# Optimization experiments

Measured on AMD Instinct MI355X. Metric: run time of the kernel, lower is better.

The kernel has to match this reference:

```python
import jax, jax.numpy as jnp
import numpy as np
from jax import lax

CHUNK = 64
KEY_DIM = 128
SCALE = KEY_DIM ** -0.5  # query scaling
EPS = 1e-06


def setup_inputs() -> dict:
    key = jax.random.key(0)
    ks = jax.random.split(key, 5)
    B, H, S, Dk, Dv = 2, 16, 4096, 128, 256
    q = jax.random.normal(ks[0], (B, H, S, Dk), jnp.float32)
    k = jax.random.normal(ks[1], (B, H, S, Dk), jnp.float32)
    v = jax.random.normal(ks[2], (B, H, S, Dv), jnp.float32)
    # decay log-gate: small negative values
    g = -0.1 * jax.random.uniform(ks[3], (B, H, S), jnp.float32)
    # delta-rule learning rate in (0, 1)
    beta = 0.05 + 0.9 * jax.random.uniform(ks[4], (B, H, S), jnp.float32)
    return {"q": q, "k": k, "v": v, "g": g, "beta": beta}


def _chunkwise(q, k, v, g, beta):
    B, H, S, Dk = q.shape
    Dv = v.shape[-1]
    L = CHUNK
    N = S // L  # S chosen as multiple of CHUNK (pad branch is a no-op)
    # L2-normalize q, k
    q = q / (jnp.linalg.norm(q, axis=-1, keepdims=True) + EPS)
    k = k / (jnp.linalg.norm(k, axis=-1, keepdims=True) + EPS)
    # chunk and move chunk axis to front for scan: [N, B, H, L, D]
    qc = jnp.transpose(q.reshape(B, H, N, L, Dk), (2, 0, 1, 3, 4))
    kc = jnp.transpose(k.reshape(B, H, N, L, Dk), (2, 0, 1, 3, 4))
    vc = jnp.transpose(v.reshape(B, H, N, L, Dv), (2, 0, 1, 3, 4))
    gc = jnp.transpose(g.reshape(B, H, N, L), (2, 0, 1, 3))
    bc = jnp.transpose(beta.reshape(B, H, N, L), (2, 0, 1, 3))

    eye = jnp.eye(L, dtype=jnp.float32)
    mask_lower = jnp.tril(jnp.ones((L, L), jnp.float32), k=-1)
    causal_mask = jnp.tril(jnp.ones((L, L), jnp.float32))

    def process_chunk(S_state, chunk_inputs):
        q_c, k_c, v_c, g_c, beta_c = chunk_inputs
        g_cum = jnp.cumsum(g_c, axis=-1)                     # [B,H,L]
        g_total = g_cum[..., -1]                             # [B,H]
        relative_gate = jnp.exp(g_cum[..., None, :] - g_cum[..., :, None])  # [B,H,L,L]
        kk = jnp.einsum('bhik,bhjk->bhij', k_c, k_c)
        M = kk * relative_gate * mask_lower
        A = eye + beta_c[..., None] * M
        diag_beta = eye * beta_c[..., None]
        T = lax.linalg.triangular_solve(A, diag_beta, left_side=True, lower=True)
        g_cum_exp = jnp.exp(g_cum)[..., None]                # [B,H,L,1]
        k_gated = k_c * g_cum_exp
        v_gated = v_c * g_cum_exp
        W = jnp.einsum('bhij,bhjk->bhik', T, k_gated)
        U = jnp.einsum('bhij,bhjv->bhiv', T, v_gated)
        O_inter = jnp.einsum('bhik,bhkv->bhiv', q_c, S_state) * g_cum_exp
        WS = jnp.einsum('bhik,bhkv->bhiv', W, S_state)
        correction = U - WS
        qk = jnp.einsum('bhik,bhjk->bhij', q_c, k_c)
        qk_gated = qk * causal_mask * relative_gate
        O_intra = jnp.einsum('bhij,bhjv->bhiv', qk_gated * SCALE, correction)
        O_chunk = O_inter * SCALE + O_intra
        S_new = S_state * jnp.exp(g_total)[..., None, None] + \
            jnp.einsum('bhik,bhiv->bhkv', k_gated, correction)
        return S_new, O_chunk

    S0 = jnp.zeros((B, H, Dk, Dv), dtype=jnp.float32)
    final_state, outputs = lax.scan(process_chunk, S0, (qc, kc, vc, gc, bc))
    output = jnp.transpose(outputs, (1, 2, 0, 3, 4)).reshape(B, H, S, Dv)
    return output.astype(q.dtype), final_state


def reference(q, k, v, g, beta):
    return _chunkwise(q, k, v, g, beta)
```

## Files before the change

### kernel.cpp

```cpp
#include <hip/hip_runtime.h>
#include <math.h>


namespace {

constexpr int kBH = 32;
constexpr int kS = 4096;
constexpr int kDk = 128;
constexpr int kDv = 256;
constexpr int kL = 64;
constexpr int kNC = kS / kL;
constexpr int kThreads = 512;
constexpr float kScale = 0.08838834764831845f;
constexpr float kEps = 1e-6f;

constexpr int KST = 136;
constexpr int TST = 72;
constexpr int SBT = 136;
constexpr int AS  = 68;

typedef __attribute__((ext_vector_type(8))) short short8;
typedef __attribute__((ext_vector_type(4))) short short4v;
typedef __attribute__((ext_vector_type(4))) float f32x4;

__device__ __forceinline__ short f2bf(float f) {
  union { float f; unsigned u; } x;
  x.f = f;
  unsigned r = x.u + 0x7fffu + ((x.u >> 16) & 1u);
  return (short)(r >> 16);
}

#define MFMA16(a, b, c) __builtin_amdgcn_mfma_f32_16x16x32_bf16((a), (b), (c), 0, 0, 0)

__global__ __launch_bounds__(kThreads, 2)
void gdn_mfma_kernel(const float* __restrict__ q, const float* __restrict__ k,
                     const float* __restrict__ v, const float* __restrict__ g,
                     const float* __restrict__ beta, float* __restrict__ out) {
  __shared__ short sKp[kL][KST];
  __shared__ short sKm[kL][KST];
  __shared__ short sQp[kL][KST];
  __shared__ short sQm[kL][KST];
  __shared__ short sTb[kL][TST];
  __shared__ short sAqk[kL][TST];
  __shared__ short sSb[32][SBT];
  __shared__ short sYT[32][TST];
  __shared__ short sCT[32][TST];
  __shared__ float sA[kL][AS];
  __shared__ float sVinv[4][16][17];
  __shared__ float sTmp[32][33];
  __shared__ float sGexp[kL], sGinv[kL], sBeta[kL];

  const int t = threadIdx.x;
  const int wave = t >> 6;
  const int lane = t & 63;
  const int n16 = lane & 15;
  const int quad = lane >> 4;
  const int r2 = t >> 3;
  const int c8 = t & 7;

  const int bh = blockIdx.x & 31;
  const int vb = blockIdx.x >> 5;

  const float* qp_g = q + (size_t)bh * kS * kDk;
  const float* kp_g = k + (size_t)bh * kS * kDk;
  const float* vp_g = v + (size_t)bh * kS * kDv + vb * 32;
  const float* gp_g = g + (size_t)bh * kS;
  const float* bp_g = beta + (size_t)bh * kS;
  float* op_g = out + (size_t)bh * kS * kDv + vb * 32;
  float* sp_g = out + (size_t)kBH * kS * kDv + (size_t)bh * kDk * kDv + vb * 32;

  for (int i = t; i < kL * TST; i += kThreads) { (&sTb[0][0])[i] = 0; (&sAqk[0][0])[i] = 0; }
  for (int i = t; i < 32 * SBT; i += kThreads) (&sSb[0][0])[i] = 0;

  f32x4 Sacc[4];
  Sacc[0] = 0; Sacc[1] = 0; Sacc[2] = 0; Sacc[3] = 0;

  for (int n = 0; n < kNC; ++n) {
    __syncthreads();

    float kv[16], qv[16], rk, rq;
    {
      const float* krow = kp_g + (size_t)(n * kL + r2) * kDk + c8 * 16;
      const float* qrow = qp_g + (size_t)(n * kL + r2) * kDk + c8 * 16;
      float ssk = 0.f, ssq = 0.f;
      #pragma unroll
      for (int m = 0; m < 4; ++m) {
        const float4 a = reinterpret_cast<const float4*>(krow)[m];
        const float4 b = reinterpret_cast<const float4*>(qrow)[m];
        kv[4*m+0]=a.x; kv[4*m+1]=a.y; kv[4*m+2]=a.z; kv[4*m+3]=a.w;
        qv[4*m+0]=b.x; qv[4*m+1]=b.y; qv[4*m+2]=b.z; qv[4*m+3]=b.w;
        ssk += a.x*a.x + a.y*a.y + a.z*a.z + a.w*a.w;
        ssq += b.x*b.x + b.y*b.y + b.z*b.z + b.w*b.w;
      }
      #pragma unroll
      for (int off = 4; off >= 1; off >>= 1) {
        ssk += __shfl_xor(ssk, off, 8);
        ssq += __shfl_xor(ssq, off, 8);
      }
      rk = 1.f / (sqrtf(ssk) + kEps);
      rq = 1.f / (sqrtf(ssq) + kEps);
    }
    if (t < kL) {
      float gv = gp_g[n * kL + t];
      float bt = bp_g[n * kL + t];
      #pragma unroll
      for (int off = 1; off < 64; off <<= 1) {
        float up = __shfl_up(gv, off, 64);
        if (lane >= off) gv += up;
      }
      sGexp[t] = __expf(gv);
      sGinv[t] = __expf(-gv);
      sBeta[t] = bt;
    }
    __syncthreads();

    {
      const float ge = sGexp[r2], gi = sGinv[r2];
      const float m_kp = rk * ge, m_km = rk * gi;
      const float m_qp = rq * ge * kScale, m_qm = rq * gi * kScale;
      short8 w0, w1;
      #pragma unroll
      for (int m = 0; m < 8; ++m) { w0[m] = f2bf(kv[m] * m_kp); w1[m] = f2bf(kv[8+m] * m_kp); }
      *(short8*)&sKp[r2][c8*16] = w0; *(short8*)&sKp[r2][c8*16+8] = w1;
      #pragma unroll
      for (int m = 0; m < 8; ++m) { w0[m] = f2bf(kv[m] * m_km); w1[m] = f2bf(kv[8+m] * m_km); }
      *(short8*)&sKm[r2][c8*16] = w0; *(short8*)&sKm[r2][c8*16+8] = w1;
      #pragma unroll
      for (int m = 0; m < 8; ++m) { w0[m] = f2bf(qv[m] * m_qp); w1[m] = f2bf(qv[8+m] * m_qp); }
      *(short8*)&sQp[r2][c8*16] = w0; *(short8*)&sQp[r2][c8*16+8] = w1;
      #pragma unroll
      for (int m = 0; m < 8; ++m) { w0[m] = f2bf(qv[m] * m_qm); w1[m] = f2bf(qv[8+m] * m_qm); }
      *(short8*)&sQm[r2][c8*16] = w0; *(short8*)&sQm[r2][c8*16+8] = w1;
    }
    __syncthreads();

    {
      const int jmax = wave & 3;
      const int i0 = (wave & 3) * 16;
      const short (*Asrc)[KST] = (wave < 4) ? sKm : sQm;
      f32x4 acc[4];
      acc[0] = 0; acc[1] = 0; acc[2] = 0; acc[3] = 0;
      #pragma unroll
      for (int ks = 0; ks < 4; ++ks) {
        short8 af = *(const short8*)&Asrc[i0 + n16][ks*32 + quad*8];
        for (int jt = 0; jt <= jmax; ++jt) {
          short8 bf = *(const short8*)&sKp[jt*16 + n16][ks*32 + quad*8];
          acc[jt] = MFMA16(af, bf, acc[jt]);
        }
      }
      if (wave < 4) {
        #pragma unroll
        for (int reg = 0; reg < 4; ++reg) {
          const int i = i0 + quad*4 + reg;
          const float bi = sBeta[i];
          for (int jt = 0; jt <= jmax; ++jt) {
            const int j = jt*16 + n16;
            if (j < i) sA[i][j] = bi * acc[jt][reg];
          }
        }
      } else {
        for (int jt = 0; jt <= jmax; ++jt) {
          #pragma unroll
          for (int reg = 0; reg < 4; ++reg) {
            const int i = i0 + quad*4 + reg, j = jt*16 + n16;
            sAqk[i][j] = (j <= i) ? f2bf(acc[jt][reg]) : (short)0;
          }
        }
      }
    }
    __syncthreads();

    f32x4 yacc[2], oacc[2];
    float vv[2][4];
    const int iy0 = (wave & 3) * 16;
    auto py_step = [&](int ks) {
      short8 ak = *(const short8*)&sKp[iy0 + n16][ks*32 + quad*8];
      short8 aq = *(const short8*)&sQp[iy0 + n16][ks*32 + quad*8];
      #pragma unroll
      for (int vt = 0; vt < 2; ++vt) {
        short8 bs = *(const short8*)&sSb[vt*16 + n16][ks*32 + quad*8];
        yacc[vt] = MFMA16(ak, bs, yacc[vt]);
        oacc[vt] = MFMA16(aq, bs, oacc[vt]);
      }
    };

    if (wave >= 4) {
      yacc[0] = 0; yacc[1] = 0; oacc[0] = 0; oacc[1] = 0;
      #pragma unroll
      for (int vt = 0; vt < 2; ++vt)
        #pragma unroll
        for (int reg = 0; reg < 4; ++reg)
          vv[vt][reg] = vp_g[(size_t)(n*kL + iy0 + quad*4 + reg) * kDv + vt*16 + n16];
      py_step(0);
    } else if (t < 64) {
      const int I = t >> 4, c = t & 15;
      float x[16];
      #pragma unroll
      for (int i = 0; i < 16; ++i) {
        float xi = (i == c) ? 1.f : 0.f;
        for (int j = 0; j < i; ++j) xi -= sA[I*16 + i][I*16 + j] * x[j];
        x[i] = xi;
      }
      const float bc = sBeta[I*16 + c];
      #pragma unroll
      for (int i = 0; i < 16; ++i) {
        sVinv[I][i][c] = x[i];
        sTb[I*16 + i][I*16 + c] = f2bf(x[i] * bc);
      }
    }
    __syncthreads();

    if (wave >= 4) {
      py_step(1);
    } else {
      const int r = t >> 4, c = t & 15;
      float m1 = 0.f, m3 = 0.f;
      #pragma unroll
      for (int kk = 0; kk < 16; ++kk) {
        m1 += sVinv[1][r][kk] * sA[16 + kk][c];
        m3 += sVinv[3][r][kk] * sA[48 + kk][32 + c];
      }
      sTmp[r][c] = m1;
      sTmp[16 + r][c] = m3;
    }
    __syncthreads();

    if (wave >= 4) {
      py_step(2);
    } else {
      const int r = t >> 4, c = t & 15;
      float x1 = 0.f, x3 = 0.f;
      #pragma unroll
      for (int kk = 0; kk < 16; ++kk) {
        x1 += sTmp[r][kk] * sVinv[0][kk][c];
        x3 += sTmp[16 + r][kk] * sVinv[2][kk][c];
      }
      x1 = -x1; x3 = -x3;
      sA[16 + r][c] = x1;
      sTb[16 + r][c] = f2bf(x1 * sBeta[c]);
      sA[48 + r][32 + c] = x3;
      sTb[48 + r][32 + c] = f2bf(x3 * sBeta[32 + c]);
    }
    __syncthreads();

    if (wave >= 4) {
      py_step(3);
    } else {
      #pragma unroll
      for (int p = 0; p < 4; ++p) {
        const int idx = t + 256*p;
        const int r = idx >> 5, c = idx & 31;
        float m = 0.f;
        if (c < 16) {
          #pragma unroll
          for (int kk = 0; kk < 16; ++kk) m += sA[32 + r][kk] * sVinv[0][kk][c];
          #pragma unroll
          for (int kk = 16; kk < 32; ++kk) m += sA[32 + r][kk] * sA[kk][c];
        } else {
          #pragma unroll
          for (int kk = 16; kk < 32; ++kk) m += sA[32 + r][kk] * sVinv[1][kk - 16][c - 16];
        }
        sTmp[r][c] = m;
      }
    }
    __syncthreads();

    if (wave >= 4) {
      #pragma unroll
      for (int vt = 0; vt < 2; ++vt) {
        short4v yw;
        #pragma unroll
        for (int reg = 0; reg < 4; ++reg) {
          const float gei = sGexp[iy0 + quad*4 + reg];
          yw[reg] = f2bf(gei * vv[vt][reg] - yacc[vt][reg]);
        }
        *(short4v*)&sYT[vt*16 + n16][iy0 + quad*4] = yw;
      }
    } else {
      #pragma unroll
      for (int p = 0; p < 4; ++p) {
        const int idx = t + 256*p;
        const int r = idx >> 5, c = idx & 31;
        float xv = 0.f;
        if (r < 16) {
          #pragma unroll
          for (int kk = 0; kk < 16; ++kk) xv += sVinv[2][r][kk] * sTmp[kk][c];
        } else {
          #pragma unroll
          for (int kk = 0; kk < 16; ++kk) xv += sA[32 + r][32 + kk] * sTmp[kk][c];
          #pragma unroll
          for (int kk = 16; kk < 32; ++kk) xv += sVinv[3][r - 16][kk - 16] * sTmp[kk][c];
        }
        sTb[32 + r][c] = f2bf(-xv * sBeta[c]);
      }
    }
    __syncthreads();

    {
      const int ic0 = (wave >> 1) * 16, vc0 = (wave & 1) * 16;
      f32x4 cacc; cacc = 0;
      #pragma unroll
      for (int ks = 0; ks < 2; ++ks) {
        short8 af = *(const short8*)&sTb[ic0 + n16][ks*32 + quad*8];
        short8 bf = *(const short8*)&sYT[vc0 + n16][ks*32 + quad*8];
        cacc = MFMA16(af, bf, cacc);
      }
      short4v cw;
      #pragma unroll
      for (int reg = 0; reg < 4; ++reg) cw[reg] = f2bf(cacc[reg]);
      *(short4v*)&sCT[vc0 + n16][ic0 + quad*4] = cw;
    }
    __syncthreads();

    if (wave >= 4) {
      const int io = (wave & 3) * 16;
      #pragma unroll
      for (int ks = 0; ks < 2; ++ks) {
        short8 af = *(const short8*)&sAqk[io + n16][ks*32 + quad*8];
        #pragma unroll
        for (int vt = 0; vt < 2; ++vt) {
          short8 bf = *(const short8*)&sCT[vt*16 + n16][ks*32 + quad*8];
          oacc[vt] = MFMA16(af, bf, oacc[vt]);
        }
      }
      #pragma unroll
      for (int vt = 0; vt < 2; ++vt)
        #pragma unroll
        for (int reg = 0; reg < 4; ++reg)
          op_g[(size_t)(n*kL + io + quad*4 + reg) * kDv + vt*16 + n16] = oacc[vt][reg];
    } else {
      const float decay = sGexp[kL - 1];
      Sacc[0] *= decay; Sacc[1] *= decay; Sacc[2] *= decay; Sacc[3] *= decay;
      #pragma unroll
      for (int a = 0; a < 2; ++a) {
        const int d0 = (wave & 3) * 32 + a * 16;
        #pragma unroll
        for (int ks = 0; ks < 2; ++ks) {
          short8 af;
          #pragma unroll
          for (int j = 0; j < 8; ++j) af[j] = sKp[ks*32 + quad*8 + j][d0 + n16];
          #pragma unroll
          for (int b = 0; b < 2; ++b) {
            short8 bf = *(const short8*)&sCT[b*16 + n16][ks*32 + quad*8];
            Sacc[a*2 + b] = MFMA16(af, bf, Sacc[a*2 + b]);
          }
        }
        #pragma unroll
        for (int b = 0; b < 2; ++b) {
          short4v sw;
          #pragma unroll
          for (int reg = 0; reg < 4; ++reg) sw[reg] = f2bf(Sacc[a*2 + b][reg]);
          *(short4v*)&sSb[b*16 + n16][d0 + quad*4] = sw;
        }
      }
    }
  }

  if (wave < 4) {
    #pragma unroll
    for (int a = 0; a < 2; ++a)
      #pragma unroll
      for (int b = 0; b < 2; ++b)
        #pragma unroll
        for (int reg = 0; reg < 4; ++reg) {
          const int d = (wave & 3) * 32 + a * 16 + quad * 4 + reg;
          sp_g[(size_t)d * kDv + b * 16 + n16] = Sacc[a*2 + b][reg];
        }
  }
}

}

extern "C" void kernel_launch(void* const* d_in, const int* in_sizes, int n_in,
                              void* d_out, int out_size, void* d_ws, size_t ws_size,
                              hipStream_t stream) {
  (void)in_sizes; (void)n_in; (void)d_ws; (void)ws_size; (void)out_size;
  const float* q    = (const float*)d_in[0];
  const float* k    = (const float*)d_in[1];
  const float* v    = (const float*)d_in[2];
  const float* g    = (const float*)d_in[3];
  const float* beta = (const float*)d_in[4];
  float* out = (float*)d_out;
  gdn_mfma_kernel<<<dim3(kBH * (kDv / 32)), dim3(kThreads), 0, stream>>>(
      q, k, v, g, beta, out);
}
```

Measured before the change: 957.0 us.

## Split value dimension into 16-wide slices and fold gates into epilogues to shrink LDS

The grid now splits Dv into 16 slices of 16 columns instead of 8 slices of 32, doubling block count, and launch bounds request 4 blocks per CU. Shared memory is cut by dropping the gated K/Q copies (Kp/Km/Qp/Qm). Only normalized K and Q are stored, and the exp(g) factors are applied in the epilogues of the A, Aqk, Y, C and output steps. Scalar arrays are aliased into padding of sA and sU, and one barrier is removed. The intent is higher occupancy and parallelism for the sequential chunk scan, at the cost of recomputing the per-chunk K/Q/T work twice as many times across blocks.

Result: slower. 1.759 ms (+83.8%).

```diff
diff --git a/kernel.cpp b/kernel.cpp
--- a/kernel.cpp
+++ b/kernel.cpp
@@ -11,6 +11,7 @@
 constexpr int kL = 64;
 constexpr int kNC = kS / kL;
 constexpr int kThreads = 512;
+constexpr int kVSlices = 16;
 constexpr float kScale = 0.08838834764831845f;
 constexpr float kEps = 1e-6f;
 
@@ -32,23 +33,25 @@
 
 #define MFMA16(a, b, c) __builtin_amdgcn_mfma_f32_16x16x32_bf16((a), (b), (c), 0, 0, 0)
 
-__global__ __launch_bounds__(kThreads, 2)
+__global__ __launch_bounds__(kThreads, 4)
 void gdn_mfma_kernel(const float* __restrict__ q, const float* __restrict__ k,
                      const float* __restrict__ v, const float* __restrict__ g,
                      const float* __restrict__ beta, float* __restrict__ out) {
-  __shared__ short sKp[kL][KST];
-  __shared__ short sKm[kL][KST];
-  __shared__ short sQp[kL][KST];
-  __shared__ short sQm[kL][KST];
-  __shared__ short sTb[kL][TST];
-  __shared__ short sAqk[kL][TST];
-  __shared__ short sSb[32][SBT];
-  __shared__ short sYT[32][TST];
-  __shared__ short sCT[32][TST];
-  __shared__ float sA[kL][AS];
-  __shared__ float sVinv[4][16][17];
-  __shared__ float sTmp[32][33];
-  __shared__ float sGexp[kL], sGinv[kL], sBeta[kL];
+  __shared__ __align__(16) short sKn[kL][KST];
+  __shared__ __align__(16) short sQn[kL][KST];
+  __shared__ __align__(16) short sTb[kL][TST];
+  __shared__ __align__(16) short sAqk[kL][TST];
+  __shared__ __align__(16) short sSb[16][SBT];
+  __shared__ __align__(16) float sA[kL][AS];
+  __shared__ __align__(16) float sU[1056];
+  __shared__ __align__(16) short sCG[16][TST];
+
+#define GEXPV(i) sA[(i) >> 4][16 + ((i) & 15)]
+#define GINVV(i) sA[4 + ((i) >> 4)][16 + ((i) & 15)]
+#define BETAV(i) sA[8 + ((i) >> 4)][16 + ((i) & 15)]
+#define SVINV(I, i, c) sA[((I) & 1) * 16 + (i)][32 + ((I) >> 1) * 17 + (c)]
+#define STMP(r, c) sU[(r) * 33 + (c)]
+  short* const sYT = (short*)sU;
 
   const int t = threadIdx.x;
   const int wave = t >> 6;
@@ -63,17 +66,19 @@
 
   const float* qp_g = q + (size_t)bh * kS * kDk;
   const float* kp_g = k + (size_t)bh * kS * kDk;
-  const float* vp_g = v + (size_t)bh * kS * kDv + vb * 32;
+  const float* vp_g = v + (size_t)bh * kS * kDv + vb * 16;
   const float* gp_g = g + (size_t)bh * kS;
   const float* bp_g = beta + (size_t)bh * kS;
-  float* op_g = out + (size_t)bh * kS * kDv + vb * 32;
-  float* sp_g = out + (size_t)kBH * kS * kDv + (size_t)bh * kDk * kDv + vb * 32;
+  float* op_g = out + (size_t)bh * kS * kDv + vb * 16;
+  float* sp_g = out + (size_t)kBH * kS * kDv + (size_t)bh * kDk * kDv + vb * 16;
 
   for (int i = t; i < kL * TST; i += kThreads) { (&sTb[0][0])[i] = 0; (&sAqk[0][0])[i] = 0; }
-  for (int i = t; i < 32 * SBT; i += kThreads) (&sSb[0][0])[i] = 0;
-
-  f32x4 Sacc[4];
-  Sacc[0] = 0; Sacc[1] = 0; Sacc[2] = 0; Sacc[3] = 0;
+  for (int i = t; i < 16 * SBT; i += kThreads) (&sSb[0][0])[i] = 0;
+
+  f32x4 Sacc[2];
+  Sacc[0] = 0; Sacc[1] = 0;
+
+  const int iy0 = (wave & 3) * 16;
 
   for (int n = 0; n < kNC; ++n) {
     __syncthreads();
@@ -108,89 +113,82 @@
         float up = __shfl_up(gv, off, 64);
         if (lane >= off) gv += up;
       }
-      sGexp[t] = __expf(gv);
-      sGinv[t] = __expf(-gv);
-      sBeta[t] = bt;
-    }
-    __syncthreads();
-
+      GEXPV(t) = __expf(gv);
+      GINVV(t) = __expf(-gv);
+      BETAV(t) = bt;
+    }
     {
-      const float ge = sGexp[r2], gi = sGinv[r2];
-      const float m_kp = rk * ge, m_km = rk * gi;
-      const float m_qp = rq * ge * kScale, m_qm = rq * gi * kScale;
+      const float mk = rk, mq = rq * kScale;
       short8 w0, w1;
       #pragma unroll
-      for (int m = 0; m < 8; ++m) { w0[m] = f2bf(kv[m] * m_kp); w1[m] = f2bf(kv[8+m] * m_kp); }
-      *(short8*)&sKp[r2][c8*16] = w0; *(short8*)&sKp[r2][c8*16+8] = w1;
-      #pragma unroll
-      for (int m = 0; m < 8; ++m) { w0[m] = f2bf(kv[m] * m_km); w1[m] = f2bf(kv[8+m] * m_km); }
-      *(short8*)&sKm[r2][c8*16] = w0; *(short8*)&sKm[r2][c8*16+8] = w1;
-      #pragma unroll
-      for (int m = 0; m < 8; ++m) { w0[m] = f2bf(qv[m] * m_qp); w1[m] = f2bf(qv[8+m] * m_qp); }
-      *(short8*)&sQp[r2][c8*16] = w0; *(short8*)&sQp[r2][c8*16+8] = w1;
-      #pragma unroll
-      for (int m = 0; m < 8; ++m) { w0[m] = f2bf(qv[m] * m_qm); w1[m] = f2bf(qv[8+m] * m_qm); }
-      *(short8*)&sQm[r2][c8*16] = w0; *(short8*)&sQm[r2][c8*16+8] = w1;
-    }
-    __syncthreads();
-
+      for (int m = 0; m < 8; ++m) { w0[m] = f2bf(kv[m] * mk); w1[m] = f2bf(kv[8+m] * mk); }
+      *(short8*)&sKn[r2][c8*16] = w0; *(short8*)&sKn[r2][c8*16+8] = w1;
+      #pragma unroll
+      for (int m = 0; m < 8; ++m) { w0[m] = f2bf(qv[m] * mq); w1[m] = f2bf(qv[8+m] * mq); }
+      *(short8*)&sQn[r2][c8*16] = w0; *(short8*)&sQn[r2][c8*16+8] = w1;
+    }
+    __syncthreads();
+
+    float vv[4];
     {
       const int jmax = wave & 3;
-      const int i0 = (wave & 3) * 16;
-      const short (*Asrc)[KST] = (wave < 4) ? sKm : sQm;
+      const short (*Asrc)[KST] = (wave < 4) ? sKn : sQn;
       f32x4 acc[4];
       acc[0] = 0; acc[1] = 0; acc[2] = 0; acc[3] = 0;
+      if (wave >= 4) {
+        #pragma unroll
+        for (int reg = 0; reg < 4; ++reg)
+          vv[reg] = vp_g[(size_t)(n*kL + iy0 + quad*4 + reg) * kDv + n16];
+      }
       #pragma unroll
       for (int ks = 0; ks < 4; ++ks) {
-        short8 af = *(const short8*)&Asrc[i0 + n16][ks*32 + quad*8];
+        short8 af = *(const short8*)&Asrc[iy0 + n16][ks*32 + quad*8];
         for (int jt = 0; jt <= jmax; ++jt) {
-          short8 bf = *(const short8*)&sKp[jt*16 + n16][ks*32 + quad*8];
+          short8 bf = *(const short8*)&sKn[jt*16 + n16][ks*32 + quad*8];
           acc[jt] = MFMA16(af, bf, acc[jt]);
         }
       }
       if (wave < 4) {
+        float sc[4];
         #pragma unroll
         for (int reg = 0; reg < 4; ++reg) {
-          const int i = i0 + quad*4 + reg;
-          const float bi = sBeta[i];
-          for (int jt = 0; jt <= jmax; ++jt) {
-            const int j = jt*16 + n16;
-            if (j < i) sA[i][j] = bi * acc[jt][reg];
+          const int i = iy0 + quad*4 + reg;
+          sc[reg] = BETAV(i) * GINVV(i);
+        }
+        for (int jt = 0; jt <= jmax; ++jt) {
+          const int j = jt*16 + n16;
+          const float gej = GEXPV(j);
+          #pragma unroll
+          for (int reg = 0; reg < 4; ++reg) {
+            const int i = iy0 + quad*4 + reg;
+            if (j < i) sA[i][j] = sc[reg] * gej * acc[jt][reg];
           }
         }
       } else {
+        float gi[4];
+        #pragma unroll
+        for (int reg = 0; reg < 4; ++reg) gi[reg] = GINVV(iy0 + quad*4 + reg);
         for (int jt = 0; jt <= jmax; ++jt) {
           #pragma unroll
           for (int reg = 0; reg < 4; ++reg) {
-            const int i = i0 + quad*4 + reg, j = jt*16 + n16;
-            sAqk[i][j] = (j <= i) ? f2bf(acc[jt][reg]) : (short)0;
+            const int i = iy0 + quad*4 + reg, j = jt*16 + n16;
+            sAqk[i][j] = (j <= i) ? f2bf(acc[jt][reg] * gi[reg]) : (short)0;
           }
         }
       }
     }
     __syncthreads();
 
-    f32x4 yacc[2], oacc[2];
-    float vv[2][4];
-    const int iy0 = (wave & 3) * 16;
+    f32x4 yacc = 0, oacc = 0;
     auto py_step = [&](int ks) {
-      short8 ak = *(const short8*)&sKp[iy0 + n16][ks*32 + quad*8];
-      short8 aq = *(const short8*)&sQp[iy0 + n16][ks*32 + quad*8];
-      #pragma unroll
-      for (int vt = 0; vt < 2; ++vt) {
-        short8 bs = *(const short8*)&sSb[vt*16 + n16][ks*32 + quad*8];
-        yacc[vt] = MFMA16(ak, bs, yacc[vt]);
-        oacc[vt] = MFMA16(aq, bs, oacc[vt]);
-      }
+      short8 ak = *(const short8*)&sKn[iy0 + n16][ks*32 + quad*8];
+      short8 aq = *(const short8*)&sQn[iy0 + n16][ks*32 + quad*8];
+      short8 bs = *(const short8*)&sSb[n16][ks*32 + quad*8];
+      yacc = MFMA16(ak, bs, yacc);
+      oacc = MFMA16(aq, bs, oacc);
     };
 
     if (wave >= 4) {
-      yacc[0] = 0; yacc[1] = 0; oacc[0] = 0; oacc[1] = 0;
-      #pragma unroll
-      for (int vt = 0; vt < 2; ++vt)
-        #pragma unroll
-        for (int reg = 0; reg < 4; ++reg)
-          vv[vt][reg] = vp_g[(size_t)(n*kL + iy0 + quad*4 + reg) * kDv + vt*16 + n16];
       py_step(0);
     } else if (t < 64) {
       const int I = t >> 4, c = t & 15;
@@ -201,10 +199,10 @@
         for (int j = 0; j < i; ++j) xi -= sA[I*16 + i][I*16 + j] * x[j];
         x[i] = xi;
       }
-      const float bc = sBeta[I*16 + c];
+      const float bc = BETAV(I*16 + c);
       #pragma unroll
       for (int i = 0; i < 16; ++i) {
-        sVinv[I][i][c] = x[i];
+        SVINV(I, i, c) = x[i];
         sTb[I*16 + i][I*16 + c] = f2bf(x[i] * bc);
       }
     }
@@ -217,11 +215,11 @@
       float m1 = 0.f, m3 = 0.f;
       #pragma unroll
       for (int kk = 0; kk < 16; ++kk) {
-        m1 += sVinv[1][r][kk] * sA[16 + kk][c];
-        m3 += sVinv[3][r][kk] * sA[48 + kk][32 + c];
-      }
-      sTmp[r][c] = m1;
-      sTmp[16 + r][c] = m3;
+        m1 += SVINV(1, r, kk) * sA[16 + kk][c];
+        m3 += SVINV(3, r, kk) * sA[48 + kk][32 + c];
+      }
+      STMP(r, c) = m1;
+      STMP(16 + r, c) = m3;
     }
     __syncthreads();
 
@@ -232,14 +230,14 @@
       float x1 = 0.f, x3 = 0.f;
       #pragma unroll
       for (int kk = 0; kk < 16; ++kk) {
-        x1 += sTmp[r][kk] * sVinv[0][kk][c];
-        x3 += sTmp[16 + r][kk] * sVinv[2][kk][c];
+        x1 += STMP(r, kk) * SVINV(0, kk, c);
+        x3 += STMP(16 + r, kk) * SVINV(2, kk, c);
       }
       x1 = -x1; x3 = -x3;
       sA[16 + r][c] = x1;
-      sTb[16 + r][c] = f2bf(x1 * sBeta[c]);
+      sTb[16 + r][c] = f2bf(x1 * BETAV(c));
       sA[48 + r][32 + c] = x3;
-      sTb[48 + r][32 + c] = f2bf(x3 * sBeta[32 + c]);
+      sTb[48 + r][32 + c] = f2bf(x3 * BETAV(32 + c));
     }
     __syncthreads();
 
@@ -253,29 +251,29 @@
         float m = 0.f;
         if (c < 16) {
           #pragma unroll
-          for (int kk = 0; kk < 16; ++kk) m += sA[32 + r][kk] * sVinv[0][kk][c];
+          for (int kk = 0; kk < 16; ++kk) m += sA[32 + r][kk] * SVINV(0, kk, c);
           #pragma unroll
           for (int kk = 16; kk < 32; ++kk) m += sA[32 + r][kk] * sA[kk][c];
         } else {
           #pragma unroll
-          for (int kk = 16; kk < 32; ++kk) m += sA[32 + r][kk] * sVinv[1][kk - 16][c - 16];
-        }
-        sTmp[r][c] = m;
-      }
-    }
-    __syncthreads();
-
-    if (wave >= 4) {
-      #pragma unroll
-      for (int vt = 0; vt < 2; ++vt) {
-        short4v yw;
-        #pragma unroll
-        for (int reg = 0; reg < 4; ++reg) {
-          const float gei = sGexp[iy0 + quad*4 + reg];
-          yw[reg] = f2bf(gei * vv[vt][reg] - yacc[vt][reg]);
-        }
-        *(short4v*)&sYT[vt*16 + n16][iy0 + quad*4] = yw;
-      }
+          for (int kk = 16; kk < 32; ++kk) m += sA[32 + r][kk] * SVINV(1, kk - 16, c - 16);
+        }
+        STMP(r, c) = m;
+      }
+    }
+    __syncthreads();
+
+    short4v yw;
+    short8 af2[2];
+    if (wave >= 4) {
+      #pragma unroll
+      for (int reg = 0; reg < 4; ++reg) {
+        const float ge = GEXPV(iy0 + quad*4 + reg);
+        yw[reg] = f2bf(ge * (vv[reg] - yacc[reg]));
+        oacc[reg] *= ge;
+      }
+      af2[0] = *(const short8*)&sAqk[iy0 + n16][quad*8];
+      af2[1] = *(const short8*)&sAqk[iy0 + n16][32 + quad*8];
     } else {
       #pragma unroll
       for (int p = 0; p < 4; ++p) {
@@ -284,74 +282,75 @@
         float xv = 0.f;
         if (r < 16) {
           #pragma unroll
-          for (int kk = 0; kk < 16; ++kk) xv += sVinv[2][r][kk] * sTmp[kk][c];
+          for (int kk = 0; kk < 16; ++kk) xv += SVINV(2, r, kk) * STMP(kk, c);
         } else {
           #pragma unroll
-          for (int kk = 0; kk < 16; ++kk) xv += sA[32 + r][32 + kk] * sTmp[kk][c];
-          #pragma unroll
-          for (int kk = 16; kk < 32; ++kk) xv += sVinv[3][r - 16][kk - 16] * sTmp[kk][c];
-        }
-        sTb[32 + r][c] = f2bf(-xv * sBeta[c]);
-      }
-    }
-    __syncthreads();
-
-    {
-      const int ic0 = (wave >> 1) * 16, vc0 = (wave & 1) * 16;
-      f32x4 cacc; cacc = 0;
-      #pragma unroll
-      for (int ks = 0; ks < 2; ++ks) {
-        short8 af = *(const short8*)&sTb[ic0 + n16][ks*32 + quad*8];
-        short8 bf = *(const short8*)&sYT[vc0 + n16][ks*32 + quad*8];
-        cacc = MFMA16(af, bf, cacc);
-      }
-      short4v cw;
-      #pragma unroll
-      for (int reg = 0; reg < 4; ++reg) cw[reg] = f2bf(cacc[reg]);
-      *(short4v*)&sCT[vc0 + n16][ic0 + quad*4] = cw;
-    }
-    __syncthreads();
-
-    if (wave >= 4) {
-      const int io = (wave & 3) * 16;
-      #pragma unroll
-      for (int ks = 0; ks < 2; ++ks) {
-        short8 af = *(const short8*)&sAqk[io + n16][ks*32 + quad*8];
-        #pragma unroll
-        for (int vt = 0; vt < 2; ++vt) {
-          short8 bf = *(const short8*)&sCT[vt*16 + n16][ks*32 + quad*8];
-          oacc[vt] = MFMA16(af, bf, oacc[vt]);
-        }
-      }
-      #pragma unroll
-      for (int vt = 0; vt < 2; ++vt)
-        #pragma unroll
-        for (int reg = 0; reg < 4; ++reg)
-          op_g[(size_t)(n*kL + io + quad*4 + reg) * kDv + vt*16 + n16] = oacc[vt][reg];
-    } else {
-      const float decay = sGexp[kL - 1];
-      Sacc[0] *= decay; Sacc[1] *= decay; Sacc[2] *= decay; Sacc[3] *= decay;
-      #pragma unroll
-      for (int a = 0; a < 2; ++a) {
-        const int d0 = (wave & 3) * 32 + a * 16;
+          for (int kk = 0; kk < 16; ++kk) xv += sA[32 + r][32 + kk] * STMP(kk, c);
+          #pragma unroll
+          for (int kk = 16; kk < 32; ++kk) xv += SVINV(3, r - 16, kk - 16) * STMP(kk, c);
+        }
+        sTb[32 + r][c] = f2bf(-xv * BETAV(c));
+      }
+    }
+    __syncthreads();
+
+    short8 afr[2][2];
+    if (wave >= 4) {
+      *(short4v*)&sYT[n16*TST + iy0 + quad*4] = yw;
+    } else {
+      const int d0b = (wave & 3) * 32;
+      #pragma unroll
+      for (int a = 0; a < 2; ++a)
         #pragma unroll
         for (int ks = 0; ks < 2; ++ks) {
           short8 af;
           #pragma unroll
-          for (int j = 0; j < 8; ++j) af[j] = sKp[ks*32 + quad*8 + j][d0 + n16];
-          #pragma unroll
-          for (int b = 0; b < 2; ++b) {
-            short8 bf = *(const short8*)&sCT[b*16 + n16][ks*32 + quad*8];
-            Sacc[a*2 + b] = MFMA16(af, bf, Sacc[a*2 + b]);
-          }
-        }
-        #pragma unroll
-        for (int b = 0; b < 2; ++b) {
-          short4v sw;
-          #pragma unroll
-          for (int reg = 0; reg < 4; ++reg) sw[reg] = f2bf(Sacc[a*2 + b][reg]);
-          *(short4v*)&sSb[b*16 + n16][d0 + quad*4] = sw;
-        }
+          for (int j = 0; j < 8; ++j)
+            af[j] = sKn[ks*32 + quad*8 + j][d0b + a*16 + n16];
+          afr[a][ks] = af;
+        }
+    }
+    __syncthreads();
+
+    if (wave < 4) {
+      f32x4 cacc = 0;
+      #pragma unroll
+      for (int ks = 0; ks < 2; ++ks) {
+        short8 af = *(const short8*)&sTb[iy0 + n16][ks*32 + quad*8];
+        short8 bf = *(const short8*)&sYT[n16*TST + ks*32 + quad*8];
+        cacc = MFMA16(af, bf, cacc);
+      }
+      short4v cw;
+      #pragma unroll
+      for (int reg = 0; reg < 4; ++reg)
+        cw[reg] = f2bf(cacc[reg] * GEXPV(iy0 + quad*4 + reg));
+      *(short4v*)&sCG[n16][iy0 + quad*4] = cw;
+    }
+    __syncthreads();
+
+    if (wave >= 4) {
+      #pragma unroll
+      for (int ks = 0; ks < 2; ++ks) {
+        short8 bf = *(const short8*)&sCG[n16][ks*32 + quad*8];
+        oacc = MFMA16(af2[ks], bf, oacc);
+      }
+      #pragma unroll
+      for (int reg = 0; reg < 4; ++reg)
+        op_g[(size_t)(n*kL + iy0 + quad*4 + reg) * kDv + n16] = oacc[reg];
+    } else {
+      const float decay = GEXPV(kL - 1);
+      Sacc[0] *= decay; Sacc[1] *= decay;
+      #pragma unroll
+      for (int a = 0; a < 2; ++a) {
+        #pragma unroll
+        for (int ks = 0; ks < 2; ++ks) {
+          short8 bf = *(const short8*)&sCG[n16][ks*32 + quad*8];
+          Sacc[a] = MFMA16(afr[a][ks], bf, Sacc[a]);
+        }
+        short4v sw;
+        #pragma unroll
+        for (int reg = 0; reg < 4; ++reg) sw[reg] = f2bf(Sacc[a][reg]);
+        *(short4v*)&sSb[n16][(wave & 3)*32 + a*16 + quad*4] = sw;
       }
     }
   }
@@ -360,13 +359,16 @@
     #pragma unroll
     for (int a = 0; a < 2; ++a)
       #pragma unroll
-      for (int b = 0; b < 2; ++b)
-        #pragma unroll
-        for (int reg = 0; reg < 4; ++reg) {
-          const int d = (wave & 3) * 32 + a * 16 + quad * 4 + reg;
-          sp_g[(size_t)d * kDv + b * 16 + n16] = Sacc[a*2 + b][reg];
-        }
+      for (int reg = 0; reg < 4; ++reg) {
+        const int d = (wave & 3)*32 + a*16 + quad*4 + reg;
+        sp_g[(size_t)d * kDv + n16] = Sacc[a][reg];
+      }
   }
+#undef GEXPV
+#undef GINVV
+#undef BETAV
+#undef SVINV
+#undef STMP
 }
 
 }
@@ -381,6 +383,6 @@
   const float* g    = (const float*)d_in[3];
   const float* beta = (const float*)d_in[4];
   float* out = (float*)d_out;
-  gdn_mfma_kernel<<<dim3(kBH * (kDv / 32)), dim3(kThreads), 0, stream>>>(
+  gdn_mfma_kernel<<<dim3(kBH * kVSlices), dim3(kThreads), 0, stream>>>(
       q, k, v, g, beta, out);
 }
```

## Software-pipeline chunk stages across wave groups with double-buffered shared memory

Applied to the files above, without the earlier changes.

Splits the block into two wave groups. Group B prepares chunk n+1 (normalization, kk/qk matmuls, triangular inverse), while group A runs the state-dependent work for chunk n (S projections, correction, output, state update). Key/query buffers and T/Aqk tiles are double-buffered, and next-chunk global loads are prefetched into registers. The gate scaling is moved out of the stored K/Q copies and applied in the epilogues, so only one bf16 copy each of K and Q is kept. The goal is to hide the serial per-chunk stages and load latency behind each other, at the cost of more shared memory, extra register pressure from prefetch buffers, and a changed bf16 rounding order.

After: 1.300 ms. +35.9%, slower.

```diff
diff --git a/kernel.cpp b/kernel.cpp
--- a/kernel.cpp
+++ b/kernel.cpp
@@ -36,27 +36,35 @@
 void gdn_mfma_kernel(const float* __restrict__ q, const float* __restrict__ k,
                      const float* __restrict__ v, const float* __restrict__ g,
                      const float* __restrict__ beta, float* __restrict__ out) {
-  __shared__ short sKp[kL][KST];
-  __shared__ short sKm[kL][KST];
-  __shared__ short sQp[kL][KST];
-  __shared__ short sQm[kL][KST];
-  __shared__ short sTb[kL][TST];
-  __shared__ short sAqk[kL][TST];
-  __shared__ short sSb[32][SBT];
-  __shared__ short sYT[32][TST];
-  __shared__ short sCT[32][TST];
-  __shared__ float sA[kL][AS];
-  __shared__ float sVinv[4][16][17];
-  __shared__ float sTmp[32][33];
-  __shared__ float sGexp[kL], sGinv[kL], sBeta[kL];
+  __shared__ __align__(16) short sKn[2][kL][KST];
+  __shared__ __align__(16) short sQn[2][kL][KST];
+  __shared__ __align__(16) short sTb[2][kL][TST];
+  __shared__ __align__(16) short sAqk[2][kL][TST];
+  __shared__ __align__(16) short sSb[32][SBT];
+  __shared__ __align__(16) float sA[kL][AS];
+  __shared__ __align__(16) float sU[1152];
+  __shared__ __align__(16) short sCG[32][TST];
+  __shared__ __align__(16) float sGe[2][kL];
+  __shared__ __align__(16) float sGi[kL];
+  __shared__ __align__(16) float sBeta[kL];
+
+#define SVINV(I, i, c) sA[((I) & 1) * 16 + (i)][32 + ((I) >> 1) * 17 + (c)]
+#define STMP(r, c) sU[(r) * 33 + (c)]
+  short* const sYT = (short*)sU;
 
   const int t = threadIdx.x;
   const int wave = t >> 6;
   const int lane = t & 63;
   const int n16 = lane & 15;
   const int quad = lane >> 4;
-  const int r2 = t >> 3;
-  const int c8 = t & 7;
+  const bool isA = (t < 256);
+  const int t2 = t & 255;
+  const int wb = wave - 4;
+  const int wa = wave & 3;
+  const int iy0 = wa * 16;
+
+  const int r2b = t2 >> 2;
+  const int cb32 = (t2 & 3) * 32;
 
   const int bh = blockIdx.x & 31;
   const int vb = blockIdx.x >> 5;
@@ -69,304 +77,361 @@
   float* op_g = out + (size_t)bh * kS * kDv + vb * 32;
   float* sp_g = out + (size_t)kBH * kS * kDv + (size_t)bh * kDk * kDv + vb * 32;
 
-  for (int i = t; i < kL * TST; i += kThreads) { (&sTb[0][0])[i] = 0; (&sAqk[0][0])[i] = 0; }
+  for (int i = t; i < 2 * kL * TST; i += kThreads) {
+    (&sTb[0][0][0])[i] = 0;
+    (&sAqk[0][0][0])[i] = 0;
+  }
   for (int i = t; i < 32 * SBT; i += kThreads) (&sSb[0][0])[i] = 0;
 
   f32x4 Sacc[4];
   Sacc[0] = 0; Sacc[1] = 0; Sacc[2] = 0; Sacc[3] = 0;
-
-  for (int n = 0; n < kNC; ++n) {
-    __syncthreads();
-
-    float kv[16], qv[16], rk, rq;
-    {
-      const float* krow = kp_g + (size_t)(n * kL + r2) * kDk + c8 * 16;
-      const float* qrow = qp_g + (size_t)(n * kL + r2) * kDk + c8 * 16;
-      float ssk = 0.f, ssq = 0.f;
-      #pragma unroll
-      for (int m = 0; m < 4; ++m) {
-        const float4 a = reinterpret_cast<const float4*>(krow)[m];
-        const float4 b = reinterpret_cast<const float4*>(qrow)[m];
-        kv[4*m+0]=a.x; kv[4*m+1]=a.y; kv[4*m+2]=a.z; kv[4*m+3]=a.w;
-        qv[4*m+0]=b.x; qv[4*m+1]=b.y; qv[4*m+2]=b.z; qv[4*m+3]=b.w;
-        ssk += a.x*a.x + a.y*a.y + a.z*a.z + a.w*a.w;
-        ssq += b.x*b.x + b.y*b.y + b.z*b.z + b.w*b.w;
-      }
-      #pragma unroll
-      for (int off = 4; off >= 1; off >>= 1) {
-        ssk += __shfl_xor(ssk, off, 8);
-        ssq += __shfl_xor(ssq, off, 8);
-      }
-      rk = 1.f / (sqrtf(ssk) + kEps);
-      rq = 1.f / (sqrtf(ssq) + kEps);
-    }
-    if (t < kL) {
-      float gv = gp_g[n * kL + t];
-      float bt = bp_g[n * kL + t];
-      #pragma unroll
-      for (int off = 1; off < 64; off <<= 1) {
-        float up = __shfl_up(gv, off, 64);
-        if (lane >= off) gv += up;
-      }
-      sGexp[t] = __expf(gv);
-      sGinv[t] = __expf(-gv);
-      sBeta[t] = bt;
-    }
-    __syncthreads();
-
-    {
-      const float ge = sGexp[r2], gi = sGinv[r2];
-      const float m_kp = rk * ge, m_km = rk * gi;
-      const float m_qp = rq * ge * kScale, m_qm = rq * gi * kScale;
-      short8 w0, w1;
-      #pragma unroll
-      for (int m = 0; m < 8; ++m) { w0[m] = f2bf(kv[m] * m_kp); w1[m] = f2bf(kv[8+m] * m_kp); }
-      *(short8*)&sKp[r2][c8*16] = w0; *(short8*)&sKp[r2][c8*16+8] = w1;
-      #pragma unroll
-      for (int m = 0; m < 8; ++m) { w0[m] = f2bf(kv[m] * m_km); w1[m] = f2bf(kv[8+m] * m_km); }
-      *(short8*)&sKm[r2][c8*16] = w0; *(short8*)&sKm[r2][c8*16+8] = w1;
-      #pragma unroll
-      for (int m = 0; m < 8; ++m) { w0[m] = f2bf(qv[m] * m_qp); w1[m] = f2bf(qv[8+m] * m_qp); }
-      *(short8*)&sQp[r2][c8*16] = w0; *(short8*)&sQp[r2][c8*16+8] = w1;
-      #pragma unroll
-      for (int m = 0; m < 8; ++m) { w0[m] = f2bf(qv[m] * m_qm); w1[m] = f2bf(qv[8+m] * m_qm); }
-      *(short8*)&sQm[r2][c8*16] = w0; *(short8*)&sQm[r2][c8*16+8] = w1;
-    }
-    __syncthreads();
-
-    {
-      const int jmax = wave & 3;
-      const int i0 = (wave & 3) * 16;
-      const short (*Asrc)[KST] = (wave < 4) ? sKm : sQm;
-      f32x4 acc[4];
-      acc[0] = 0; acc[1] = 0; acc[2] = 0; acc[3] = 0;
+  f32x4 yacc[2], oacc[2];
+  float vv[2][4];
+  float4 kv4[8], qv4[8];
+  float gv0 = 0.f, bt0 = 0.f;
+
+  if (!isA) {
+    const float* krow = kp_g + (size_t)r2b * kDk + cb32;
+    const float* qrow = qp_g + (size_t)r2b * kDk + cb32;
+    #pragma unroll
+    for (int m = 0; m < 8; ++m) {
+      kv4[m] = reinterpret_cast<const float4*>(krow)[m];
+      qv4[m] = reinterpret_cast<const float4*>(qrow)[m];
+    }
+    if (wb == 0) { gv0 = gp_g[lane]; bt0 = bp_g[lane]; }
+  }
+
+  for (int it = 0; it <= kNC; ++it) {
+    const int cbuf = it & 1;
+    const int pbuf = cbuf ^ 1;
+    const bool doA = (it > 0);
+    const bool doB = (it < kNC);
+
+    if (doB) {
+      if (wave == 4) {
+        float gv = gv0;
+        #pragma unroll
+        for (int off = 1; off < 64; off <<= 1) {
+          float up = __shfl_up(gv, off, 64);
+          if (lane >= off) gv += up;
+        }
+        sGe[cbuf][lane] = __expf(gv);
+        sGi[lane] = __expf(-gv);
+        sBeta[lane] = bt0;
+      }
+      if (!isA) {
+        float ssk = 0.f, ssq = 0.f;
+        #pragma unroll
+        for (int m = 0; m < 8; ++m) {
+          ssk += kv4[m].x * kv4[m].x + kv4[m].y * kv4[m].y +
+                 kv4[m].z * kv4[m].z + kv4[m].w * kv4[m].w;
+          ssq += qv4[m].x * qv4[m].x + qv4[m].y * qv4[m].y +
+                 qv4[m].z * qv4[m].z + qv4[m].w * qv4[m].w;
+        }
+        ssk += __shfl_xor(ssk, 1, 4); ssk += __shfl_xor(ssk, 2, 4);
+        ssq += __shfl_xor(ssq, 1, 4); ssq += __shfl_xor(ssq, 2, 4);
+        const float mk = 1.f / (sqrtf(ssk) + kEps);
+        const float mq = kScale / (sqrtf(ssq) + kEps);
+        #pragma unroll
+        for (int m = 0; m < 4; ++m) {
+          const float4 a = kv4[2 * m], b2 = kv4[2 * m + 1];
+          short8 w;
+          w[0] = f2bf(a.x * mk);  w[1] = f2bf(a.y * mk);
+          w[2] = f2bf(a.z * mk);  w[3] = f2bf(a.w * mk);
+          w[4] = f2bf(b2.x * mk); w[5] = f2bf(b2.y * mk);
+          w[6] = f2bf(b2.z * mk); w[7] = f2bf(b2.w * mk);
+          *(short8*)&sKn[cbuf][r2b][cb32 + m * 8] = w;
+        }
+        #pragma unroll
+        for (int m = 0; m < 4; ++m) {
+          const float4 a = qv4[2 * m], b2 = qv4[2 * m + 1];
+          short8 w;
+          w[0] = f2bf(a.x * mq);  w[1] = f2bf(a.y * mq);
+          w[2] = f2bf(a.z * mq);  w[3] = f2bf(a.w * mq);
+          w[4] = f2bf(b2.x * mq); w[5] = f2bf(b2.y * mq);
+          w[6] = f2bf(b2.z * mq); w[7] = f2bf(b2.w * mq);
+          *(short8*)&sQn[cbuf][r2b][cb32 + m * 8] = w;
+        }
+      }
+    }
+    if (doA && isA) {
+      yacc[0] = 0; yacc[1] = 0; oacc[0] = 0; oacc[1] = 0;
       #pragma unroll
       for (int ks = 0; ks < 4; ++ks) {
-        short8 af = *(const short8*)&Asrc[i0 + n16][ks*32 + quad*8];
-        for (int jt = 0; jt <= jmax; ++jt) {
-          short8 bf = *(const short8*)&sKp[jt*16 + n16][ks*32 + quad*8];
-          acc[jt] = MFMA16(af, bf, acc[jt]);
-        }
-      }
-      if (wave < 4) {
+        short8 ak = *(const short8*)&sKn[pbuf][iy0 + n16][ks * 32 + quad * 8];
+        short8 aq = *(const short8*)&sQn[pbuf][iy0 + n16][ks * 32 + quad * 8];
+        #pragma unroll
+        for (int vt = 0; vt < 2; ++vt) {
+          short8 bs = *(const short8*)&sSb[vt * 16 + n16][ks * 32 + quad * 8];
+          yacc[vt] = MFMA16(ak, bs, yacc[vt]);
+          oacc[vt] = MFMA16(aq, bs, oacc[vt]);
+        }
+      }
+      #pragma unroll
+      for (int vt = 0; vt < 2; ++vt) {
+        short4v yw;
         #pragma unroll
         for (int reg = 0; reg < 4; ++reg) {
-          const int i = i0 + quad*4 + reg;
-          const float bi = sBeta[i];
-          for (int jt = 0; jt <= jmax; ++jt) {
-            const int j = jt*16 + n16;
-            if (j < i) sA[i][j] = bi * acc[jt][reg];
+          const float ge = sGe[pbuf][iy0 + quad * 4 + reg];
+          yw[reg] = f2bf(ge * (vv[vt][reg] - yacc[vt][reg]));
+          oacc[vt][reg] *= ge;
+        }
+        *(short4v*)&sYT[(vt * 16 + n16) * TST + iy0 + quad * 4] = yw;
+      }
+    }
+    __syncthreads();
+
+    if (doB && !isA) {
+      f32x4 kacc[4], qacc[4];
+      #pragma unroll
+      for (int j = 0; j < 4; ++j) { kacc[j] = 0; qacc[j] = 0; }
+      const int ik = wb * 16;
+      const int iq = (3 - wb) * 16;
+      #pragma unroll
+      for (int ks = 0; ks < 4; ++ks) {
+        short8 akk = *(const short8*)&sKn[cbuf][ik + n16][ks * 32 + quad * 8];
+        short8 aqq = *(const short8*)&sQn[cbuf][iq + n16][ks * 32 + quad * 8];
+        #pragma unroll
+        for (int jt = 0; jt < 4; ++jt) {
+          short8 bf = *(const short8*)&sKn[cbuf][jt * 16 + n16][ks * 32 + quad * 8];
+          if (jt <= wb)     kacc[jt] = MFMA16(akk, bf, kacc[jt]);
+          if (jt <= 3 - wb) qacc[jt] = MFMA16(aqq, bf, qacc[jt]);
+        }
+      }
+      {
+        float sc[4];
+        #pragma unroll
+        for (int reg = 0; reg < 4; ++reg) {
+          const int i = ik + quad * 4 + reg;
+          sc[reg] = sBeta[i] * sGi[i];
+        }
+        #pragma unroll
+        for (int jt = 0; jt < 4; ++jt) {
+          if (jt <= wb) {
+            const int j = jt * 16 + n16;
+            const float gej = sGe[cbuf][j];
+            #pragma unroll
+            for (int reg = 0; reg < 4; ++reg) {
+              const int i = ik + quad * 4 + reg;
+              if (j < i) sA[i][j] = sc[reg] * gej * kacc[jt][reg];
+            }
           }
         }
-      } else {
-        for (int jt = 0; jt <= jmax; ++jt) {
-          #pragma unroll
-          for (int reg = 0; reg < 4; ++reg) {
-            const int i = i0 + quad*4 + reg, j = jt*16 + n16;
-            sAqk[i][j] = (j <= i) ? f2bf(acc[jt][reg]) : (short)0;
+      }
+      {
+        float gi4[4];
+        #pragma unroll
+        for (int reg = 0; reg < 4; ++reg) gi4[reg] = sGi[iq + quad * 4 + reg];
+        #pragma unroll
+        for (int jt = 0; jt < 4; ++jt) {
+          if (jt <= 3 - wb) {
+            #pragma unroll
+            for (int reg = 0; reg < 4; ++reg) {
+              const int i = iq + quad * 4 + reg, j = jt * 16 + n16;
+              sAqk[cbuf][i][j] = (j <= i) ? f2bf(qacc[jt][reg] * gi4[reg]) : (short)0;
+            }
           }
         }
       }
     }
-    __syncthreads();
-
-    f32x4 yacc[2], oacc[2];
-    float vv[2][4];
-    const int iy0 = (wave & 3) * 16;
-    auto py_step = [&](int ks) {
-      short8 ak = *(const short8*)&sKp[iy0 + n16][ks*32 + quad*8];
-      short8 aq = *(const short8*)&sQp[iy0 + n16][ks*32 + quad*8];
+    if (doA && isA) {
       #pragma unroll
       for (int vt = 0; vt < 2; ++vt) {
-        short8 bs = *(const short8*)&sSb[vt*16 + n16][ks*32 + quad*8];
-        yacc[vt] = MFMA16(ak, bs, yacc[vt]);
-        oacc[vt] = MFMA16(aq, bs, oacc[vt]);
-      }
-    };
-
-    if (wave >= 4) {
-      yacc[0] = 0; yacc[1] = 0; oacc[0] = 0; oacc[1] = 0;
+        f32x4 cacc = 0;
+        #pragma unroll
+        for (int ks = 0; ks < 2; ++ks) {
+          short8 af = *(const short8*)&sTb[pbuf][iy0 + n16][ks * 32 + quad * 8];
+          short8 bf = *(const short8*)&sYT[(vt * 16 + n16) * TST + ks * 32 + quad * 8];
+          cacc = MFMA16(af, bf, cacc);
+        }
+        short4v cw;
+        #pragma unroll
+        for (int reg = 0; reg < 4; ++reg)
+          cw[reg] = f2bf(cacc[reg] * sGe[pbuf][iy0 + quad * 4 + reg]);
+        *(short4v*)&sCG[vt * 16 + n16][iy0 + quad * 4] = cw;
+      }
+    }
+    __syncthreads();
+
+    if (isA && it < kNC) {
       #pragma unroll
       for (int vt = 0; vt < 2; ++vt)
         #pragma unroll
         for (int reg = 0; reg < 4; ++reg)
-          vv[vt][reg] = vp_g[(size_t)(n*kL + iy0 + quad*4 + reg) * kDv + vt*16 + n16];
-      py_step(0);
-    } else if (t < 64) {
-      const int I = t >> 4, c = t & 15;
+          vv[vt][reg] = vp_g[(size_t)(it * kL + iy0 + quad * 4 + reg) * kDv +
+                             vt * 16 + n16];
+    }
+    if (!isA && it + 1 < kNC) {
+      const float* krow = kp_g + (size_t)((it + 1) * kL + r2b) * kDk + cb32;
+      const float* qrow = qp_g + (size_t)((it + 1) * kL + r2b) * kDk + cb32;
+      #pragma unroll
+      for (int m = 0; m < 8; ++m) {
+        kv4[m] = reinterpret_cast<const float4*>(krow)[m];
+        qv4[m] = reinterpret_cast<const float4*>(qrow)[m];
+      }
+      if (wb == 0) {
+        gv0 = gp_g[(it + 1) * kL + lane];
+        bt0 = bp_g[(it + 1) * kL + lane];
+      }
+    }
+    if (doB && wave == 4) {
+      const int I = lane >> 4, c = lane & 15;
       float x[16];
       #pragma unroll
       for (int i = 0; i < 16; ++i) {
         float xi = (i == c) ? 1.f : 0.f;
-        for (int j = 0; j < i; ++j) xi -= sA[I*16 + i][I*16 + j] * x[j];
+        for (int j = 0; j < i; ++j) xi -= sA[I * 16 + i][I * 16 + j] * x[j];
         x[i] = xi;
       }
-      const float bc = sBeta[I*16 + c];
+      const float bc = sBeta[I * 16 + c];
       #pragma unroll
       for (int i = 0; i < 16; ++i) {
-        sVinv[I][i][c] = x[i];
-        sTb[I*16 + i][I*16 + c] = f2bf(x[i] * bc);
-      }
-    }
-    __syncthreads();
-
-    if (wave >= 4) {
-      py_step(1);
-    } else {
-      const int r = t >> 4, c = t & 15;
+        SVINV(I, i, c) = x[i];
+        sTb[cbuf][I * 16 + i][I * 16 + c] = f2bf(x[i] * bc);
+      }
+    }
+    if (doA && isA) {
+      #pragma unroll
+      for (int ks = 0; ks < 2; ++ks) {
+        short8 af = *(const short8*)&sAqk[pbuf][iy0 + n16][ks * 32 + quad * 8];
+        #pragma unroll
+        for (int vt = 0; vt < 2; ++vt) {
+          short8 bf = *(const short8*)&sCG[vt * 16 + n16][ks * 32 + quad * 8];
+          oacc[vt] = MFMA16(af, bf, oacc[vt]);
+        }
+      }
+      #pragma unroll
+      for (int vt = 0; vt < 2; ++vt)
+        #pragma unroll
+        for (int reg = 0; reg < 4; ++reg)
+          op_g[(size_t)((it - 1) * kL + iy0 + quad * 4 + reg) * kDv +
+               vt * 16 + n16] = oacc[vt][reg];
+    }
+    __syncthreads();
+
+    short8 afr[2][2];
+    if (doB && !isA) {
+      const int r = t2 >> 4, c = t2 & 15;
       float m1 = 0.f, m3 = 0.f;
       #pragma unroll
       for (int kk = 0; kk < 16; ++kk) {
-        m1 += sVinv[1][r][kk] * sA[16 + kk][c];
-        m3 += sVinv[3][r][kk] * sA[48 + kk][32 + c];
-      }
-      sTmp[r][c] = m1;
-      sTmp[16 + r][c] = m3;
-    }
-    __syncthreads();
-
-    if (wave >= 4) {
-      py_step(2);
-    } else {
-      const int r = t >> 4, c = t & 15;
+        m1 += SVINV(1, r, kk) * sA[16 + kk][c];
+        m3 += SVINV(3, r, kk) * sA[48 + kk][32 + c];
+      }
+      STMP(r, c) = m1;
+      STMP(16 + r, c) = m3;
+    }
+    if (doA && isA) {
+      const float decay = sGe[pbuf][kL - 1];
+      Sacc[0] *= decay; Sacc[1] *= decay; Sacc[2] *= decay; Sacc[3] *= decay;
+      const int d0b = wa * 32;
+      #pragma unroll
+      for (int a = 0; a < 2; ++a)
+        #pragma unroll
+        for (int ks = 0; ks < 2; ++ks) {
+          short8 af;
+          #pragma unroll
+          for (int j = 0; j < 8; ++j)
+            af[j] = sKn[pbuf][ks * 32 + quad * 8 + j][d0b + a * 16 + n16];
+          afr[a][ks] = af;
+        }
+    }
+    __syncthreads();
+
+    if (doB && !isA) {
+      const int r = t2 >> 4, c = t2 & 15;
       float x1 = 0.f, x3 = 0.f;
       #pragma unroll
       for (int kk = 0; kk < 16; ++kk) {
-        x1 += sTmp[r][kk] * sVinv[0][kk][c];
-        x3 += sTmp[16 + r][kk] * sVinv[2][kk][c];
+        x1 += STMP(r, kk) * SVINV(0, kk, c);
+        x3 += STMP(16 + r, kk) * SVINV(2, kk, c);
       }
       x1 = -x1; x3 = -x3;
       sA[16 + r][c] = x1;
-      sTb[16 + r][c] = f2bf(x1 * sBeta[c]);
+      sTb[cbuf][16 + r][c] = f2bf(x1 * sBeta[c]);
       sA[48 + r][32 + c] = x3;
-      sTb[48 + r][32 + c] = f2bf(x3 * sBeta[32 + c]);
-    }
-    __syncthreads();
-
-    if (wave >= 4) {
-      py_step(3);
-    } else {
+      sTb[cbuf][48 + r][32 + c] = f2bf(x3 * sBeta[32 + c]);
+    }
+    if (doA && isA) {
+      const int d0b = wa * 32;
+      #pragma unroll
+      for (int a = 0; a < 2; ++a) {
+        #pragma unroll
+        for (int ks = 0; ks < 2; ++ks) {
+          #pragma unroll
+          for (int b = 0; b < 2; ++b) {
+            short8 bf = *(const short8*)&sCG[b * 16 + n16][ks * 32 + quad * 8];
+            Sacc[a * 2 + b] = MFMA16(afr[a][ks], bf, Sacc[a * 2 + b]);
+          }
+        }
+        #pragma unroll
+        for (int b = 0; b < 2; ++b) {
+          short4v sw;
+          #pragma unroll
+          for (int reg = 0; reg < 4; ++reg) sw[reg] = f2bf(Sacc[a * 2 + b][reg]);
+          *(short4v*)&sSb[b * 16 + n16][d0b + a * 16 + quad * 4] = sw;
+        }
+      }
+    }
+    __syncthreads();
+
+    if (doB && !isA) {
       #pragma unroll
       for (int p = 0; p < 4; ++p) {
-        const int idx = t + 256*p;
+        const int idx = t2 + 256 * p;
         const int r = idx >> 5, c = idx & 31;
         float m = 0.f;
         if (c < 16) {
           #pragma unroll
-          for (int kk = 0; kk < 16; ++kk) m += sA[32 + r][kk] * sVinv[0][kk][c];
+          for (int kk = 0; kk < 16; ++kk) m += sA[32 + r][kk] * SVINV(0, kk, c);
           #pragma unroll
           for (int kk = 16; kk < 32; ++kk) m += sA[32 + r][kk] * sA[kk][c];
         } else {
           #pragma unroll
-          for (int kk = 16; kk < 32; ++kk) m += sA[32 + r][kk] * sVinv[1][kk - 16][c - 16];
-        }
-        sTmp[r][c] = m;
-      }
-    }
-    __syncthreads();
-
-    if (wave >= 4) {
-      #pragma unroll
-      for (int vt = 0; vt < 2; ++vt) {
-        short4v yw;
-        #pragma unroll
-        for (int reg = 0; reg < 4; ++reg) {
-          const float gei = sGexp[iy0 + quad*4 + reg];
-          yw[reg] = f2bf(gei * vv[vt][reg] - yacc[vt][reg]);
-        }
-        *(short4v*)&sYT[vt*16 + n16][iy0 + quad*4] = yw;
-      }
-    } else {
+          for (int kk = 16; kk < 32; ++kk)
+            m += sA[32 + r][kk] * SVINV(1, kk - 16, c - 16);
+        }
+        STMP(r, c) = m;
+      }
+    }
+    __syncthreads();
+
+    if (doB && !isA) {
       #pragma unroll
       for (int p = 0; p < 4; ++p) {
-        const int idx = t + 256*p;
+        const int idx = t2 + 256 * p;
         const int r = idx >> 5, c = idx & 31;
         float xv = 0.f;
         if (r < 16) {
           #pragma unroll
-          for (int kk = 0; kk < 16; ++kk) xv += sVinv[2][r][kk] * sTmp[kk][c];
+          for (int kk = 0; kk < 16; ++kk) xv += SVINV(2, r, kk) * STMP(kk, c);
         } else {
           #pragma unroll
-          for (int kk = 0; kk < 16; ++kk) xv += sA[32 + r][32 + kk] * sTmp[kk][c];
-          #pragma unroll
-          for (int kk = 16; kk < 32; ++kk) xv += sVinv[3][r - 16][kk - 16] * sTmp[kk][c];
-        }
-        sTb[32 + r][c] = f2bf(-xv * sBeta[c]);
-      }
-    }
-    __syncthreads();
-
-    {
-      const int ic0 = (wave >> 1) * 16, vc0 = (wave & 1) * 16;
-      f32x4 cacc; cacc = 0;
-      #pragma unroll
-      for (int ks = 0; ks < 2; ++ks) {
-        short8 af = *(const short8*)&sTb[ic0 + n16][ks*32 + quad*8];
-        short8 bf = *(const short8*)&sYT[vc0 + n16][ks*32 + quad*8];
-        cacc = MFMA16(af, bf, cacc);
-      }
-      short4v cw;
-      #pragma unroll
-      for (int reg = 0; reg < 4; ++reg) cw[reg] = f2bf(cacc[reg]);
-      *(short4v*)&sCT[vc0 + n16][ic0 + quad*4] = cw;
-    }
-    __syncthreads();
-
-    if (wave >= 4) {
-      const int io = (wave & 3) * 16;
-      #pragma unroll
-      for (int ks = 0; ks < 2; ++ks) {
-        short8 af = *(const short8*)&sAqk[io + n16][ks*32 + quad*8];
-        #pragma unroll
-        for (int vt = 0; vt < 2; ++vt) {
-          short8 bf = *(const short8*)&sCT[vt*16 + n16][ks*32 + quad*8];
-          oacc[vt] = MFMA16(af, bf, oacc[vt]);
-        }
-      }
-      #pragma unroll
-      for (int vt = 0; vt < 2; ++vt)
-        #pragma unroll
-        for (int reg = 0; reg < 4; ++reg)
-          op_g[(size_t)(n*kL + io + quad*4 + reg) * kDv + vt*16 + n16] = oacc[vt][reg];
-    } else {
-      const float decay = sGexp[kL - 1];
-      Sacc[0] *= decay; Sacc[1] *= decay; Sacc[2] *= decay; Sacc[3] *= decay;
-      #pragma unroll
-      for (int a = 0; a < 2; ++a) {
-        const int d0 = (wave & 3) * 32 + a * 16;
-        #pragma unroll
-        for (int ks = 0; ks < 2; ++ks) {
-          short8 af;
-          #pragma unroll
-          for (int j = 0; j < 8; ++j) af[j] = sKp[ks*32 + quad*8 + j][d0 + n16];
-          #pragma unroll
-          for (int b = 0; b < 2; ++b) {
-            short8 bf = *(const short8*)&sCT[b*16 + n16][ks*32 + quad*8];
-            Sacc[a*2 + b] = MFMA16(af, bf, Sacc[a*2 + b]);
-          }
-        }
-        #pragma unroll
-        for (int b = 0; b < 2; ++b) {
-          short4v sw;
-          #pragma unroll
-          for (int reg = 0; reg < 4; ++reg) sw[reg] = f2bf(Sacc[a*2 + b][reg]);
-          *(short4v*)&sSb[b*16 + n16][d0 + quad*4] = sw;
-        }
-      }
-    }
+          for (int kk = 0; kk < 16; ++kk) xv += sA[32 + r][32 + kk] * STMP(kk, c);
+          #pragma unroll
+          for (int kk = 16; kk < 32; ++kk)
+            xv += SVINV(3, r - 16, kk - 16) * STMP(kk, c);
+        }
+        sTb[cbuf][32 + r][c] = f2bf(-xv * sBeta[c]);
+      }
+    }
+    __syncthreads();
   }
 
-  if (wave < 4) {
+  if (isA) {
+    const int d0b = wa * 32;
     #pragma unroll
     for (int a = 0; a < 2; ++a)
       #pragma unroll
       for (int b = 0; b < 2; ++b)
         #pragma unroll
         for (int reg = 0; reg < 4; ++reg) {
-          const int d = (wave & 3) * 32 + a * 16 + quad * 4 + reg;
-          sp_g[(size_t)d * kDv + b * 16 + n16] = Sacc[a*2 + b][reg];
+          const int d = d0b + a * 16 + quad * 4 + reg;
+          sp_g[(size_t)d * kDv + b * 16 + n16] = Sacc[a * 2 + b][reg];
         }
   }
+#undef SVINV
+#undef STMP
 }
 
 }
```
